# Performance work log

Measured on AMD Instinct MI355X. Metric: run time of the kernel, lower is better.

The kernel has to match this reference:

```python
import jax, jax.numpy as jnp
import numpy as np

# norse LIF/LI defaults
DT = 1e-3
TAU_SYN_INV = 200.0
TAU_MEM_INV = 100.0
V_TH = 1.0
V_LEAK = 0.0
V_RESET = 0.0
ALPHA = 100.0  # SuperSpike surrogate slope ('super' method)
N_CLASSES = 10


@jax.custom_vjp
def spike(x):
    # heaviside forward, SuperSpike surrogate backward
    return (x > 0).astype(x.dtype)

def _spike_fwd(x):
    return spike(x), x

def _spike_bwd(x, g):
    return (g / (ALPHA * jnp.abs(x) + 1.0) ** 2,)

spike.defvjp(_spike_fwd, _spike_bwd)


def conv2d(x, w, b):
    y = jax.lax.conv_general_dilated(x, w, (1, 1), 'VALID',
                                     dimension_numbers=('NCHW', 'OIHW', 'NCHW'))
    return y + b[None, :, None, None]


def maxpool2(x):
    return jax.lax.reduce_window(x, -jnp.inf, jax.lax.max,
                                 (1, 1, 2, 2), (1, 1, 2, 2), 'VALID')


def lif_step(inp, v, i):
    # norse lif_feed_forward_step
    v_dec = v + DT * TAU_MEM_INV * ((V_LEAK - v) + i)
    i_dec = i * (1.0 - DT * TAU_SYN_INV)
    z = spike(v_dec - V_TH)
    v_new = (1.0 - z) * v_dec + z * V_RESET
    i_new = i_dec + inp
    return z, v_new, i_new


def setup_inputs() -> dict:
    key = jax.random.key(0)
    ks = jax.random.split(key, 9)
    T, B, C, H = 32, 32, 1, 64
    feats = 13 * 13 * 32  # 5408
    return {
        'x': jax.random.normal(ks[0], (T, B, C, H, H), jnp.float32),
        'conv1_w': jax.random.normal(ks[1], (16, 1, 5, 5), jnp.float32) * 0.2,
        'conv1_b': jax.random.normal(ks[2], (16,), jnp.float32) * 0.1,
        'conv2_w': jax.random.normal(ks[3], (32, 16, 5, 5), jnp.float32) * 0.05,
        'conv2_b': jax.random.normal(ks[4], (32,), jnp.float32) * 0.1,
        'fc1_w': jax.random.normal(ks[5], (500, feats), jnp.float32) * 0.02,
        'fc1_b': jax.random.normal(ks[6], (500,), jnp.float32) * 0.1,
        'out_w': jax.random.normal(ks[7], (10, 500), jnp.float32) * 0.06,
    }


def reference(x, conv1_w, conv1_b, conv2_w, conv2_b, fc1_w, fc1_b, out_w):
    B = x.shape[1]
    zeros = lambda s: jnp.zeros(s, x.dtype)
    init = ((zeros((B, 16, 60, 60)), zeros((B, 16, 60, 60))),
            (zeros((B, 32, 26, 26)), zeros((B, 32, 26, 26))),
            (zeros((B, 500)), zeros((B, 500))),
            (zeros((B, N_CLASSES)), zeros((B, N_CLASSES))))

    def step(state, xt):
        (v0, i0), (v1, i1), (v2, i2), (vo, io) = state
        z = conv2d(xt, conv1_w, conv1_b)                     # [B,16,60,60]
        z, v0, i0 = lif_step(z, v0, i0)
        z = maxpool2(z)                                      # [B,16,30,30]
        z = N_CLASSES * conv2d(z, conv2_w, conv2_b)          # [B,32,26,26]
        z, v1, i1 = lif_step(z, v1, i1)
        z = maxpool2(z).reshape(B, -1)                       # [B,5408]
        z = z @ fc1_w.T + fc1_b                              # [B,500]
        z, v2, i2 = lif_step(z, v2, i2)
        zr = jax.nn.relu(z)
        # LI (non-spiking) linear readout cell: norse li_step, no bias
        v_out = vo + DT * TAU_MEM_INV * ((V_LEAK - vo) + io)
        io = io * (1.0 - DT * TAU_SYN_INV) + zr @ out_w.T
        return ((v0, i0), (v1, i1), (v2, i2), (v_out, io)), v_out

    _, voltages = jax.lax.scan(step, init, x)
    return voltages  # [T, B, n_classes]
```

## Files before the change

kernel.cpp:

```cpp
#include <hip/hip_runtime.h>


#define T_STEPS 32

typedef __bf16 bf16x8 __attribute__((ext_vector_type(8)));
typedef float f32x16 __attribute__((ext_vector_type(16)));
typedef int i32x4 __attribute__((ext_vector_type(4)));

__device__ __forceinline__ int xcd_swz(int orig, int nwg) {
    const int q = nwg >> 3, r = nwg & 7;
    const int xcd = orig & 7, idx = orig >> 3;
    return (xcd < r ? xcd * (q + 1) : r * (q + 1) + (xcd - r) * q) + idx;
}

__global__ __launch_bounds__(256) void k_tr(
    const float* __restrict__ x, float* __restrict__ xT)
{
    const int y = blockIdx.x, t = blockIdx.y;
    const int tid = threadIdx.x;
    __shared__ float tile[32][65];

    const int lx = tid & 63, bg = tid >> 6;
    #pragma unroll
    for (int p = 0; p < 8; ++p) {
        const int b = bg + p * 4;
        tile[b][lx] = x[((size_t)(t * 32 + b) * 64 + y) * 64 + lx];
    }
    __syncthreads();
    const int wb = tid & 31, xg = tid >> 5;
    #pragma unroll
    for (int p = 0; p < 8; ++p) {
        const int xx = xg + p * 8;
        xT[((size_t)(t * 64 + y) * 64 + xx) * 32 + wb] = tile[wb][xx];
    }
}

__global__ __launch_bounds__(256) void k1_conv1(
    const float* __restrict__ xT,
    const float* __restrict__ w1,
    const float* __restrict__ b1,
    unsigned short* __restrict__ zp1c)
{
    const int pos = xcd_swz(blockIdx.x, 900);
    const int bhalf = blockIdx.y;
    const int py = pos / 30, px = pos % 30;
    const int y0 = 2 * py, x0 = 2 * px;
    const int tid = threadIdx.x;
    const int b = tid & 31, slot = tid >> 5;
    const int co = bhalf * 8 + slot;

    __shared__ float ws[200];
    __shared__ float win[1152];
    for (int i = tid; i < 200; i += 256) ws[i] = w1[bhalf * 200 + i];
    const float bias = b1[co];
    const float* __restrict__ wc = ws + slot * 25;

    float v[4] = {0.f,0.f,0.f,0.f};
    float cu[4] = {0.f,0.f,0.f,0.f};

    const size_t obase = (size_t)bhalf * 230400 + (size_t)pos * 256
                       + (slot >> 1) * 64 + b * 2 + (slot & 1);

    for (int t = 0; t < T_STEPS; ++t) {
        __syncthreads();
        {
            const float4* __restrict__ src0 =
                (const float4*)(xT + ((size_t)(t * 64 + y0) * 64 + x0) * 32);
            float4* __restrict__ dst = (float4*)win;
            for (int i = tid; i < 288; i += 256) {
                const int r = i / 48, j = i - r * 48;
                dst[r * 48 + j] = src0[r * 512 + j];
            }
        }
        __syncthreads();

        float xr[36];
        #pragma unroll
        for (int rc = 0; rc < 36; ++rc) xr[rc] = win[rc * 32 + b];

        float acc[4] = {0.f, 0.f, 0.f, 0.f};
        #pragma unroll
        for (int ky = 0; ky < 5; ++ky) {
            #pragma unroll
            for (int kx = 0; kx < 5; ++kx) {
                const float w = wc[ky * 5 + kx];
                acc[0] = fmaf(w, xr[ky * 6 + kx],           acc[0]);
                acc[1] = fmaf(w, xr[ky * 6 + kx + 1],       acc[1]);
                acc[2] = fmaf(w, xr[(ky + 1) * 6 + kx],     acc[2]);
                acc[3] = fmaf(w, xr[(ky + 1) * 6 + kx + 1], acc[3]);
            }
        }

        float zmax = 0.f;
        #pragma unroll
        for (int q = 0; q < 4; ++q) {
            const float inp = acc[q] + bias;
            const float vv = v[q], cur = cu[q];
            const float vd = vv + 0.1f * (cur - vv);
            const float id = 0.8f * cur;
            const float z = (vd - 1.0f > 0.0f) ? 1.0f : 0.0f;
            v[q] = (z > 0.f) ? 0.f : vd;
            cu[q] = id + inp;
            zmax = fmaxf(zmax, z);
        }
        zp1c[(size_t)t * 460800 + obase] =
            (unsigned short)(__float_as_uint(zmax) >> 16);
    }
}

__global__ __launch_bounds__(256) void k2w_split(
    const float* __restrict__ w2, unsigned short* __restrict__ wsplit)
{
    const int i = blockIdx.x * 256 + threadIdx.x;
    if (i >= 12800) return;
    const int co = i / 400, rest = i % 400;
    const int ci = rest / 25, tap = rest % 25;
    const float w = w2[i];
    const unsigned wb = __float_as_uint(w);
    const unsigned hi = wb & 0xFFFF0000u;
    const float r1 = w - __uint_as_float(hi);
    const unsigned mid = __float_as_uint(r1) & 0xFFFF0000u;
    const float r2 = r1 - __uint_as_float(mid);
    const unsigned lo = __float_as_uint(r2) & 0xFFFF0000u;
    const int base = (tap * 32 + co) * 16 + ci;
    wsplit[base]         = (unsigned short)(hi >> 16);
    wsplit[12800 + base] = (unsigned short)(mid >> 16);
    wsplit[25600 + base] = (unsigned short)(lo >> 16);
}

__global__ __launch_bounds__(256, 2) void k2a_mfma(
    const unsigned* __restrict__ zp1c,
    const unsigned short* __restrict__ wsplit,
    float* __restrict__ raw)
{
    __shared__ i32x4 wlds[4800];
    const int tid = threadIdx.x;
    for (int i = tid; i < 4800; i += 256)
        wlds[i] = ((const i32x4*)wsplit)[i];
    __syncthreads();

    const int w = tid >> 6, l = tid & 63;
    const int task = xcd_swz(blockIdx.x, 1352) * 4 + w;
    const int t = task / 169, pg = task % 169;
    const int py = pg / 13, px = pg % 13;
    const int b = l & 31, cig = l >> 5;
    const int abase = (l & 31) * 2 + cig;

    const unsigned* __restrict__ zt =
        zp1c + (size_t)(t * 2 + cig) * 115200 + ((2 * py) * 30 + 2 * px) * 128 + b;

    f32x16 accA, accB, accC, accD;
    #pragma unroll
    for (int r = 0; r < 16; ++r) { accA[r] = 0.f; accB[r] = 0.f; accC[r] = 0.f; accD[r] = 0.f; }

    #pragma unroll
    for (int wy = 0; wy < 6; ++wy) {
        i32x4 bw[6];
        #pragma unroll
        for (int wx = 0; wx < 6; ++wx) {
            const unsigned* __restrict__ c = zt + (wy * 30 + wx) * 128;
            bw[wx][0] = (int)c[0];
            bw[wx][1] = (int)c[32];
            bw[wx][2] = (int)c[64];
            bw[wx][3] = (int)c[96];
        }
        if (wy <= 4) {
            #pragma unroll
            for (int sp = 0; sp < 3; ++sp) {
                #pragma unroll
                for (int kx = 0; kx < 5; ++kx) {
                    const int tap = wy * 5 + kx;
                    const bf16x8 A = __builtin_bit_cast(bf16x8, wlds[(sp * 25 + tap) * 64 + abase]);
                    accA = __builtin_amdgcn_mfma_f32_32x32x16_bf16(
                        A, __builtin_bit_cast(bf16x8, bw[kx]),     accA, 0, 0, 0);
                    accB = __builtin_amdgcn_mfma_f32_32x32x16_bf16(
                        A, __builtin_bit_cast(bf16x8, bw[kx + 1]), accB, 0, 0, 0);
                }
            }
        }
        if (wy >= 1) {
            #pragma unroll
            for (int sp = 0; sp < 3; ++sp) {
                #pragma unroll
                for (int kx = 0; kx < 5; ++kx) {
                    const int tap = (wy - 1) * 5 + kx;
                    const bf16x8 A = __builtin_bit_cast(bf16x8, wlds[(sp * 25 + tap) * 64 + abase]);
                    accC = __builtin_amdgcn_mfma_f32_32x32x16_bf16(
                        A, __builtin_bit_cast(bf16x8, bw[kx]),     accC, 0, 0, 0);
                    accD = __builtin_amdgcn_mfma_f32_32x32x16_bf16(
                        A, __builtin_bit_cast(bf16x8, bw[kx + 1]), accD, 0, 0, 0);
                }
            }
        }
    }

    float* __restrict__ rp = raw + (size_t)(t * 169 + pg) * 4096 + b;
    const int hi = l >> 5;
    #pragma unroll
    for (int r = 0; r < 16; ++r) {
        const int row = (r & 3) + 8 * (r >> 2) + 4 * hi;
        rp[row * 32]        = accA[r];
        rp[1024 + row * 32] = accB[r];
        rp[2048 + row * 32] = accC[r];
        rp[3072 + row * 32] = accD[r];
    }
}

__global__ __launch_bounds__(256) void k2b_lifpool(
    const float* __restrict__ raw,
    const float* __restrict__ b2,
    unsigned short* __restrict__ zb)
{
    const int bid = blockIdx.x;
    const int pg = bid >> 2, cog = bid & 3;
    const int tid = threadIdx.x;
    const int co = cog * 8 + (tid >> 5), b = tid & 31;
    const float bias = b2[co];
    const float* __restrict__ rp = raw + (size_t)pg * 4096 + co * 32 + b;

    const int k = co * 169 + pg;
    const size_t zidx0 = ((size_t)((k >> 4) * 2 + ((k >> 3) & 1)) * 32 + b) * 8 + (k & 7);

    float v0=0.f,v1=0.f,v2=0.f,v3=0.f, c0=0.f,c1=0.f,c2=0.f,c3=0.f;
    for (int t = 0; t < T_STEPS; ++t) {
        const float* __restrict__ r = rp + (size_t)t * 692224;
        float zm = 0.f;
        { const float inp = 10.f*(r[0]    + bias); const float vd = v0 + 0.1f*(c0-v0);
          const float z = (vd-1.f>0.f)?1.f:0.f; v0 = (z>0.f)?0.f:vd; c0 = 0.8f*c0 + inp;
          zm = fmaxf(zm, z); }
        { const float inp = 10.f*(r[1024] + bias); const float vd = v1 + 0.1f*(c1-v1);
          const float z = (vd-1.f>0.f)?1.f:0.f; v1 = (z>0.f)?0.f:vd; c1 = 0.8f*c1 + inp;
          zm = fmaxf(zm, z); }
        { const float inp = 10.f*(r[2048] + bias); const float vd = v2 + 0.1f*(c2-v2);
          const float z = (vd-1.f>0.f)?1.f:0.f; v2 = (z>0.f)?0.f:vd; c2 = 0.8f*c2 + inp;
          zm = fmaxf(zm, z); }
        { const float inp = 10.f*(r[3072] + bias); const float vd = v3 + 0.1f*(c3-v3);
          const float z = (vd-1.f>0.f)?1.f:0.f; v3 = (z>0.f)?0.f:vd; c3 = 0.8f*c3 + inp;
          zm = fmaxf(zm, z); }
        zb[(size_t)t * 173056 + zidx0] =
            (unsigned short)(__float_as_uint(zm) >> 16);
    }
}

__global__ __launch_bounds__(256) void k3w_split(
    const float* __restrict__ fw, unsigned short* __restrict__ wf)
{
    const int gid = blockIdx.x * 256 + threadIdx.x;
    const int l = gid & 31;
    const int ks = (gid >> 5) % 338;
    const int nt = gid / 10816;
    const int n = nt * 32 + l;

    unsigned hipk[8], midpk[8], lopk[8];
    #pragma unroll
    for (int p = 0; p < 8; ++p) {
        unsigned h[2], m[2], o[2];
        #pragma unroll
        for (int e = 0; e < 2; ++e) {
            const float w = (n < 500) ? fw[(size_t)n * 5408 + ks * 16 + 2 * p + e] : 0.f;
            const unsigned wb = __float_as_uint(w);
            const unsigned hi = wb & 0xFFFF0000u;
            const float r1 = w - __uint_as_float(hi);
            const unsigned mid = __float_as_uint(r1) & 0xFFFF0000u;
            const float r2 = r1 - __uint_as_float(mid);
            h[e] = hi >> 16; m[e] = mid >> 16; o[e] = __float_as_uint(r2) >> 16;
        }
        hipk[p]  = h[0] | (h[1] << 16);
        midpk[p] = m[0] | (m[1] << 16);
        lopk[p]  = o[0] | (o[1] << 16);
    }

    i32x4* __restrict__ wv = (i32x4*)wf;
    const int base = (nt * 338 + ks) * 64 + l * 2;
    i32x4 a, bq;
    a[0]=(int)hipk[0];a[1]=(int)hipk[1];a[2]=(int)hipk[2];a[3]=(int)hipk[3];
    bq[0]=(int)hipk[4];bq[1]=(int)hipk[5];bq[2]=(int)hipk[6];bq[3]=(int)hipk[7];
    wv[base] = a; wv[base + 1] = bq;
    a[0]=(int)midpk[0];a[1]=(int)midpk[1];a[2]=(int)midpk[2];a[3]=(int)midpk[3];
    bq[0]=(int)midpk[4];bq[1]=(int)midpk[5];bq[2]=(int)midpk[6];bq[3]=(int)midpk[7];
    wv[base + 346112] = a; wv[base + 346113] = bq;
    a[0]=(int)lopk[0];a[1]=(int)lopk[1];a[2]=(int)lopk[2];a[3]=(int)lopk[3];
    bq[0]=(int)lopk[4];bq[1]=(int)lopk[5];bq[2]=(int)lopk[6];bq[3]=(int)lopk[7];
    wv[base + 692224] = a; wv[base + 692225] = bq;
}

__global__ __launch_bounds__(256) void k3_mfma(
    const unsigned short* __restrict__ wf,
    const unsigned short* __restrict__ zb,
    float* __restrict__ part)
{
    const int wgid = xcd_swz(blockIdx.x, 416);
    const int ntg = wgid / 52, rest = wgid % 52;
    const int kc = rest >> 2, cgg = rest & 3;
    const int tid = threadIdx.x;
    const int w = tid >> 6, l = tid & 63;
    const int nt = ntg * 2 + (w >> 1);
    const int cg = cgg * 2 + (w & 1);
    const int lo5 = l & 31, hi1 = l >> 5;

    const i32x4* __restrict__ wv = (const i32x4*)wf;
    const i32x4* __restrict__ zv = (const i32x4*)zb;

    f32x16 acc0, acc1, acc2, acc3;
    #pragma unroll
    for (int r = 0; r < 16; ++r) { acc0[r]=0.f; acc1[r]=0.f; acc2[r]=0.f; acc3[r]=0.f; }

    const int ks0 = kc * 26;
    #pragma unroll 2
    for (int kk = 0; kk < 26; ++kk) {
        const int ks = ks0 + kk;
        const int ab = (nt * 338 + ks) * 64 + lo5 * 2 + hi1;
        const bf16x8 A0 = __builtin_bit_cast(bf16x8, wv[ab]);
        const bf16x8 A1 = __builtin_bit_cast(bf16x8, wv[ab + 346112]);
        const bf16x8 A2 = __builtin_bit_cast(bf16x8, wv[ab + 692224]);
        const int b0 = (((cg * 4) * 338 + ks) * 2 + hi1) * 32 + lo5;
        const bf16x8 B0 = __builtin_bit_cast(bf16x8, zv[b0]);
        const bf16x8 B1 = __builtin_bit_cast(bf16x8, zv[b0 + 21632]);
        const bf16x8 B2 = __builtin_bit_cast(bf16x8, zv[b0 + 43264]);
        const bf16x8 B3 = __builtin_bit_cast(bf16x8, zv[b0 + 64896]);
        acc0 = __builtin_amdgcn_mfma_f32_32x32x16_bf16(A0, B0, acc0, 0, 0, 0);
        acc1 = __builtin_amdgcn_mfma_f32_32x32x16_bf16(A0, B1, acc1, 0, 0, 0);
        acc2 = __builtin_amdgcn_mfma_f32_32x32x16_bf16(A0, B2, acc2, 0, 0, 0);
        acc3 = __builtin_amdgcn_mfma_f32_32x32x16_bf16(A0, B3, acc3, 0, 0, 0);
        acc0 = __builtin_amdgcn_mfma_f32_32x32x16_bf16(A1, B0, acc0, 0, 0, 0);
        acc1 = __builtin_amdgcn_mfma_f32_32x32x16_bf16(A1, B1, acc1, 0, 0, 0);
        acc2 = __builtin_amdgcn_mfma_f32_32x32x16_bf16(A1, B2, acc2, 0, 0, 0);
        acc3 = __builtin_amdgcn_mfma_f32_32x32x16_bf16(A1, B3, acc3, 0, 0, 0);
        acc0 = __builtin_amdgcn_mfma_f32_32x32x16_bf16(A2, B0, acc0, 0, 0, 0);
        acc1 = __builtin_amdgcn_mfma_f32_32x32x16_bf16(A2, B1, acc1, 0, 0, 0);
        acc2 = __builtin_amdgcn_mfma_f32_32x32x16_bf16(A2, B2, acc2, 0, 0, 0);
        acc3 = __builtin_amdgcn_mfma_f32_32x32x16_bf16(A2, B3, acc3, 0, 0, 0);
    }

    float* __restrict__ pp = part + ((size_t)(kc * 512 + nt * 32)) * 1024 + cg * 128 + lo5;
    #pragma unroll
    for (int r = 0; r < 16; ++r) {
        const int row = (r & 3) + 8 * (r >> 2) + 4 * hi1;
        pp[row * 1024]      = acc0[r];
        pp[row * 1024 + 32] = acc1[r];
        pp[row * 1024 + 64] = acc2[r];
        pp[row * 1024 + 96] = acc3[r];
    }
}

__global__ __launch_bounds__(256) void k3b_lif(
    const float* __restrict__ part,
    const float* __restrict__ fb,
    float* __restrict__ za)
{
    const int idx = blockIdx.x * 256 + threadIdx.x;
    if (idx >= 16000) return;
    const int n = idx >> 5, b = idx & 31;
    const float bias = fb[n];

    float v = 0.f, cu = 0.f;
    for (int t = 0; t < T_STEPS; ++t) {
        float s = 0.f;
        #pragma unroll
        for (int p = 0; p < 13; ++p)
            s += part[(size_t)p * 524288 + n * 1024 + t * 32 + b];
        s += bias;

        const float vd = v + 0.1f * (cu - v);
        const float id = 0.8f * cu;
        const float z = (vd - 1.0f > 0.0f) ? 1.0f : 0.0f;
        v = (z > 0.f) ? 0.f : vd;
        cu = id + s;
        za[(size_t)t * 16000 + idx] = z;
    }
}

__global__ __launch_bounds__(256) void k4_dot(
    const float* __restrict__ za,
    const float* __restrict__ ow,
    float* __restrict__ dota)
{
    const int c = blockIdx.x, t = blockIdx.y;
    const int tid = threadIdx.x;
    const int b = tid & 31, nc = tid >> 5;
    const float* __restrict__ wr = ow + c * 500;
    const float* __restrict__ zt = za + (size_t)t * 16000;

    float acc = 0.f;
    for (int j = 0; j < 63; ++j) {
        const int n = nc * 63 + j;
        if (n < 500) acc = fmaf(zt[n * 32 + b], wr[n], acc);
    }

    __shared__ float red[256];
    red[tid] = acc;
    __syncthreads();
    if (tid < 32) {
        float dot = 0.f;
        #pragma unroll
        for (int q = 0; q < 8; ++q) dot += red[q * 32 + tid];
        dota[((size_t)t * 10 + c) * 32 + tid] = dot;
    }
}

__global__ __launch_bounds__(320) void k5_li(
    const float* __restrict__ dota,
    float* __restrict__ outp)
{
    const int tid = threadIdx.x;
    if (tid >= 320) return;
    const int c = tid / 32, b = tid & 31;

    float vo = 0.f, io = 0.f;
    for (int t = 0; t < T_STEPS; ++t) {
        const float vout = vo + 0.1f * (io - vo);
        outp[t * 320 + b * 10 + c] = vout;
        vo = vout;
        io = 0.8f * io + dota[(t * 10 + c) * 32 + b];
    }
}

extern "C" void kernel_launch(void* const* d_in, const int* in_sizes, int n_in,
                              void* d_out, int out_size, void* d_ws, size_t ws_size,
                              hipStream_t stream) {
    const float* x  = (const float*)d_in[0];
    const float* w1 = (const float*)d_in[1];
    const float* b1 = (const float*)d_in[2];
    const float* w2 = (const float*)d_in[3];
    const float* b2 = (const float*)d_in[4];
    const float* fw = (const float*)d_in[5];
    const float* fb = (const float*)d_in[6];
    const float* ow = (const float*)d_in[7];
    float* out = (float*)d_out;
    float* ws = (float*)d_ws;

    size_t off = 0;
    float* zp1a = ws + off; off += 14745600;
    float* za   = ws + off; off += 512000;
    float* dota = ws + off; off += 10240;
    unsigned short* wsplit = (unsigned short*)(ws + off); off += 19200;
    float* big  = ws + off; off += 22151168;

    float* xT       = big;
    float* conv2raw = big;
    float* part     = big;
    unsigned short* zp1c = (unsigned short*)zp1a;
    unsigned short* zb = (unsigned short*)zp1a;
    unsigned short* wf = (unsigned short*)(zp1a + 4194304);

    k2w_split<<<50, 256, 0, stream>>>(w2, wsplit);
    k_tr     <<<dim3(64, 32), 256, 0, stream>>>(x, xT);
    k1_conv1 <<<dim3(900, 2), 256, 0, stream>>>(xT, w1, b1, zp1c);
    k2a_mfma <<<1352, 256, 0, stream>>>((const unsigned*)zp1c, wsplit, conv2raw);
    k2b_lifpool<<<676, 256, 0, stream>>>(conv2raw, b2, zb);
    k3w_split<<<676, 256, 0, stream>>>(fw, wf);
    k3_mfma  <<<416, 256, 0, stream>>>(wf, zb, part);
    k3b_lif  <<<63, 256, 0, stream>>>(part, fb, za);
    k4_dot   <<<dim3(10, 32), 256, 0, stream>>>(za, ow, dota);
    k5_li    <<<1, 320, 0, stream>>>(dota, out);
}
```

Baseline: 241.8 us.

## Register-block conv1 over four channels per thread with double-buffered input window

The conv1+LIF kernel now computes four output channels per thread, with weights held in registers. It launches one 128-thread block per pooled position instead of two 256-thread blocks split by channel half, so each input window is loaded once per position rather than twice. The shared-memory input window is double-buffered so the next timestep's load overlaps compute, which removes one barrier per step. Spike outputs are packed two bf16 values per 32-bit store. In exchange, register pressure rises sharply (100 weight plus 32 state registers) and the grid has fewer threads, so occupancy may drop.

```diff
diff --git a/kernel.cpp b/kernel.cpp
--- a/kernel.cpp
+++ b/kernel.cpp
@@ -35,76 +35,113 @@
     }
 }
 
-__global__ __launch_bounds__(256) void k1_conv1(
+__global__ __launch_bounds__(128) void k1_conv1(
     const float* __restrict__ xT,
     const float* __restrict__ w1,
     const float* __restrict__ b1,
-    unsigned short* __restrict__ zp1c)
+    unsigned* __restrict__ zp1c)
 {
     const int pos = xcd_swz(blockIdx.x, 900);
-    const int bhalf = blockIdx.y;
     const int py = pos / 30, px = pos % 30;
     const int y0 = 2 * py, x0 = 2 * px;
     const int tid = threadIdx.x;
     const int b = tid & 31, slot = tid >> 5;
-    const int co = bhalf * 8 + slot;
-
-    __shared__ float ws[200];
-    __shared__ float win[1152];
-    for (int i = tid; i < 200; i += 256) ws[i] = w1[bhalf * 200 + i];
-    const float bias = b1[co];
-    const float* __restrict__ wc = ws + slot * 25;
-
-    float v[4] = {0.f,0.f,0.f,0.f};
-    float cu[4] = {0.f,0.f,0.f,0.f};
-
-    const size_t obase = (size_t)bhalf * 230400 + (size_t)pos * 256
-                       + (slot >> 1) * 64 + b * 2 + (slot & 1);
+
+    __shared__ float win[2][1152];
+
+    float wreg[4][25];
+    float bias[4];
+    #pragma unroll
+    for (int j = 0; j < 4; ++j) {
+        const int co = slot * 4 + j;
+        bias[j] = b1[co];
+        #pragma unroll
+        for (int k = 0; k < 25; ++k) wreg[j][k] = w1[co * 25 + k];
+    }
+
+    float v[4][4], cu[4][4];
+    #pragma unroll
+    for (int j = 0; j < 4; ++j)
+        #pragma unroll
+        for (int q = 0; q < 4; ++q) { v[j][q] = 0.f; cu[j][q] = 0.f; }
+
+    const int cig = slot >> 1;
+    const int pair0 = (slot & 1) * 2;
+    const size_t sbase = (size_t)cig * 115200 + (size_t)pos * 128 + pair0 * 32 + b;
+
+    {
+        const float4* __restrict__ src =
+            (const float4*)(xT + ((size_t)y0 * 64 + x0) * 32);
+        float4* __restrict__ dst = (float4*)win[0];
+        for (int i = tid; i < 288; i += 128) {
+            const int r = i / 48, jj = i - r * 48;
+            dst[r * 48 + jj] = src[r * 512 + jj];
+        }
+    }
 
     for (int t = 0; t < T_STEPS; ++t) {
         __syncthreads();
-        {
-            const float4* __restrict__ src0 =
-                (const float4*)(xT + ((size_t)(t * 64 + y0) * 64 + x0) * 32);
-            float4* __restrict__ dst = (float4*)win;
-            for (int i = tid; i < 288; i += 256) {
-                const int r = i / 48, j = i - r * 48;
-                dst[r * 48 + j] = src0[r * 512 + j];
+        if (t + 1 < T_STEPS) {
+            const float4* __restrict__ src =
+                (const float4*)(xT + ((size_t)((t + 1) * 64 + y0) * 64 + x0) * 32);
+            float4* __restrict__ dst = (float4*)win[(t + 1) & 1];
+            for (int i = tid; i < 288; i += 128) {
+                const int r = i / 48, jj = i - r * 48;
+                dst[r * 48 + jj] = src[r * 512 + jj];
             }
         }
-        __syncthreads();
-
+
+        const float* __restrict__ cur = win[t & 1];
         float xr[36];
         #pragma unroll
-        for (int rc = 0; rc < 36; ++rc) xr[rc] = win[rc * 32 + b];
-
-        float acc[4] = {0.f, 0.f, 0.f, 0.f};
+        for (int rc = 0; rc < 36; ++rc) xr[rc] = cur[rc * 32 + b];
+
+        float acc[4][4];
+        #pragma unroll
+        for (int j = 0; j < 4; ++j)
+            #pragma unroll
+            for (int q = 0; q < 4; ++q) acc[j][q] = 0.f;
+
         #pragma unroll
         for (int ky = 0; ky < 5; ++ky) {
             #pragma unroll
             for (int kx = 0; kx < 5; ++kx) {
-                const float w = wc[ky * 5 + kx];
-                acc[0] = fmaf(w, xr[ky * 6 + kx],           acc[0]);
-                acc[1] = fmaf(w, xr[ky * 6 + kx + 1],       acc[1]);
-                acc[2] = fmaf(w, xr[(ky + 1) * 6 + kx],     acc[2]);
-                acc[3] = fmaf(w, xr[(ky + 1) * 6 + kx + 1], acc[3]);
+                const int tap = ky * 5 + kx;
+                const float e00 = xr[ky * 6 + kx];
+                const float e01 = xr[ky * 6 + kx + 1];
+                const float e10 = xr[(ky + 1) * 6 + kx];
+                const float e11 = xr[(ky + 1) * 6 + kx + 1];
+                #pragma unroll
+                for (int j = 0; j < 4; ++j) {
+                    const float w = wreg[j][tap];
+                    acc[j][0] = fmaf(w, e00, acc[j][0]);
+                    acc[j][1] = fmaf(w, e01, acc[j][1]);
+                    acc[j][2] = fmaf(w, e10, acc[j][2]);
+                    acc[j][3] = fmaf(w, e11, acc[j][3]);
+                }
             }
         }
 
-        float zmax = 0.f;
-        #pragma unroll
-        for (int q = 0; q < 4; ++q) {
-            const float inp = acc[q] + bias;
-            const float vv = v[q], cur = cu[q];
-            const float vd = vv + 0.1f * (cur - vv);
-            const float id = 0.8f * cur;
-            const float z = (vd - 1.0f > 0.0f) ? 1.0f : 0.0f;
-            v[q] = (z > 0.f) ? 0.f : vd;
-            cu[q] = id + inp;
-            zmax = fmaxf(zmax, z);
-        }
-        zp1c[(size_t)t * 460800 + obase] =
-            (unsigned short)(__float_as_uint(zmax) >> 16);
+        unsigned zbits[4];
+        #pragma unroll
+        for (int j = 0; j < 4; ++j) {
+            float zmax = 0.f;
+            #pragma unroll
+            for (int q = 0; q < 4; ++q) {
+                const float inp = acc[j][q] + bias[j];
+                const float vv = v[j][q], curr = cu[j][q];
+                const float vd = vv + 0.1f * (curr - vv);
+                const float id = 0.8f * curr;
+                const float z = (vd - 1.0f > 0.0f) ? 1.0f : 0.0f;
+                v[j][q] = (z > 0.f) ? 0.f : vd;
+                cu[j][q] = id + inp;
+                zmax = fmaxf(zmax, z);
+            }
+            zbits[j] = __float_as_uint(zmax) >> 16;
+        }
+        unsigned* __restrict__ op = zp1c + (size_t)t * 230400 + sbase;
+        op[0]  = zbits[0] | (zbits[1] << 16);
+        op[32] = zbits[2] | (zbits[3] << 16);
     }
 }
 
@@ -439,14 +476,14 @@
     float* xT       = big;
     float* conv2raw = big;
     float* part     = big;
-    unsigned short* zp1c = (unsigned short*)zp1a;
+    unsigned* zp1c = (unsigned*)zp1a;
     unsigned short* zb = (unsigned short*)zp1a;
     unsigned short* wf = (unsigned short*)(zp1a + 4194304);
 
     k2w_split<<<50, 256, 0, stream>>>(w2, wsplit);
     k_tr     <<<dim3(64, 32), 256, 0, stream>>>(x, xT);
-    k1_conv1 <<<dim3(900, 2), 256, 0, stream>>>(xT, w1, b1, zp1c);
-    k2a_mfma <<<1352, 256, 0, stream>>>((const unsigned*)zp1c, wsplit, conv2raw);
+    k1_conv1 <<<900, 128, 0, stream>>>(xT, w1, b1, zp1c);
+    k2a_mfma <<<1352, 256, 0, stream>>>(zp1c, wsplit, conv2raw);
     k2b_lifpool<<<676, 256, 0, stream>>>(conv2raw, b2, zb);
     k3w_split<<<676, 256, 0, stream>>>(fw, wf);
     k3_mfma  <<<416, 256, 0, stream>>>(wf, zb, part);
```

Result: slower. 281.1 us (+16.2%).
